# Optimization experiments

Hardware: AMD Instinct MI355X
Metric: run time of the kernel (lower is better)

Reference implementation:

```python
import jax, jax.numpy as jnp
import numpy as np

EPS = 1e-5

def _dynconv(x, w):
    # x: [B,C,H,W], w: [B,O,C,1,1] -> per-sample 1x1 conv == batched matmul
    return jnp.einsum('bchw,boc->bohw', x, w[:, :, :, 0, 0])

def _instance_norm(x):
    # InstanceNorm2d(affine=False): normalize over HxW per (b,c), biased var
    m = jnp.mean(x, axis=(2, 3), keepdims=True)
    v = jnp.var(x, axis=(2, 3), keepdims=True)
    return (x - m) / jnp.sqrt(v + EPS)

def setup_inputs() -> dict:
    key = jax.random.key(0)
    ks = jax.random.split(key, 10)
    B, C, O = 16, 128, 128
    hs = [128, 64, 32, 16, 8]
    inp = {}
    for i, h in enumerate(hs):
        inp[f'x{i+1}'] = jax.random.normal(ks[i], (B, C, h, h), dtype=jnp.float32)
        inp[f'l{i+1}fs'] = jax.random.normal(ks[5 + i], (B, O, C, 1, 1), dtype=jnp.float32)
    return inp

def reference(x1, x2, x3, x4, x5, l1fs, l2fs, l3fs, l4fs, l5fs):
    y1 = _instance_norm(_dynconv(x1, l1fs))
    y2 = _instance_norm(_dynconv(x2, l2fs))
    y3 = _instance_norm(_dynconv(x3, l3fs))
    y4 = _instance_norm(_dynconv(x4, l4fs))
    y5 = _dynconv(x5, l5fs)  # x5 is not normalized in the original
    return (y1, y2, y3, y4, y5)
```

## Files before the change

### kernel.cpp

```cpp
#include <hip/hip_runtime.h>
#include <hip/hip_bf16.h>

typedef float f32x4 __attribute__((ext_vector_type(4)));
typedef short s16x8 __attribute__((ext_vector_type(8)));
typedef short s16x4 __attribute__((ext_vector_type(4)));

static __device__ __forceinline__ short f2bf(float f) {
  union { __hip_bfloat16 h; short s; } u;
  u.h = __float2bfloat16(f);
  return u.s;
}
static __device__ __forceinline__ float bf2f(short s) {
  union { unsigned u; float f; } v;
  v.u = ((unsigned)(unsigned short)s) << 16;
  return v.f;
}
static __device__ __forceinline__ unsigned pack2(float a, float b) {
  return ((unsigned)(unsigned short)f2bf(a)) | (((unsigned)(unsigned short)f2bf(b)) << 16);
}
static __device__ __forceinline__ s16x8 pack8(f32x4 v0, f32x4 v1) {
  s16x8 r;
  r[0] = f2bf(v0.x); r[1] = f2bf(v0.y); r[2] = f2bf(v0.z); r[3] = f2bf(v0.w);
  r[4] = f2bf(v1.x); r[5] = f2bf(v1.y); r[6] = f2bf(v1.z); r[7] = f2bf(v1.w);
  return r;
}

#define GRAW_SZ   (4 * 16 * 16384)
#define MX_BASE   GRAW_SZ
#define MX_SZ     (4 * 16 * 128)
#define MEAN_BASE (MX_BASE + MX_SZ)
#define RSTD_BASE (MEAN_BASE + MX_SZ)

__global__ __launch_bounds__(256, 3) void k_gram(
    const float* __restrict__ x0, const float* __restrict__ x1,
    const float* __restrict__ x2, const float* __restrict__ x3,
    float* __restrict__ graw, float* __restrict__ mxraw) {
  const int bid = blockIdx.x;
  const float* xp; int s, b, ch, L; long long N;
  if (bid < 512)      { s = 0; b = bid >> 5; ch = bid & 31; xp = x0; N = 16384; L = 512; }
  else if (bid < 640) { int r = bid - 512; s = 1; b = r >> 3; ch = r & 7; xp = x1; N = 4096; L = 512; }
  else if (bid < 672) { int r = bid - 640; s = 2; b = r >> 1; ch = r & 1; xp = x2; N = 1024; L = 512; }
  else                { int r = bid - 672; s = 3; b = r;      ch = 0;     xp = x3; N = 256;  L = 256; }
  const int rounds = L >> 5;
  const int t = threadIdx.x;
  const int lane = t & 63, wv = t >> 6;
  const int wm = wv >> 1, wn = wv & 1;
  const int l15 = lane & 15, quad = lane >> 4;

  f32x4 acc[4][4];
  #pragma unroll
  for (int i = 0; i < 4; ++i)
    #pragma unroll
    for (int j = 0; j < 4; ++j) { f32x4 z = {0.f,0.f,0.f,0.f}; acc[i][j] = z; }
  float mxp[4] = {0.f, 0.f, 0.f, 0.f};

  const float* xb = xp + (long long)b * 128 * N + (long long)ch * L;
  const float* aptr[4]; const float* bptr[4];
  #pragma unroll
  for (int i = 0; i < 4; ++i)
    aptr[i] = xb + (long long)(wm * 64 + i * 16 + l15) * N + quad * 8;
  #pragma unroll
  for (int j = 0; j < 4; ++j)
    bptr[j] = xb + (long long)(wn * 64 + j * 16 + l15) * N + quad * 8;

  for (int r = 0; r < rounds; ++r) {
    const int k0 = r << 5;
    s16x8 af[4], bfq[4];
    #pragma unroll
    for (int i = 0; i < 4; ++i) {
      f32x4 v0 = *(const f32x4*)(aptr[i] + k0);
      f32x4 v1 = *(const f32x4*)(aptr[i] + k0 + 4);
      if (wn == 0)
        mxp[i] += (v0.x + v0.y + v0.z + v0.w) + (v1.x + v1.y + v1.z + v1.w);
      af[i] = pack8(v0, v1);
    }
    if (wm == wn) {
      #pragma unroll
      for (int j = 0; j < 4; ++j) bfq[j] = af[j];
    } else {
      #pragma unroll
      for (int j = 0; j < 4; ++j) {
        f32x4 v0 = *(const f32x4*)(bptr[j] + k0);
        f32x4 v1 = *(const f32x4*)(bptr[j] + k0 + 4);
        bfq[j] = pack8(v0, v1);
      }
    }
    #pragma unroll
    for (int i = 0; i < 4; ++i)
      #pragma unroll
      for (int j = 0; j < 4; ++j)
        acc[i][j] = __builtin_amdgcn_mfma_f32_16x16x32_bf16(af[i], bfq[j], acc[i][j], 0, 0, 0);
  }

  float* G = graw + (long long)(s * 16 + b) * 16384;
  #pragma unroll
  for (int i = 0; i < 4; ++i) {
    #pragma unroll
    for (int rr = 0; rr < 4; ++rr) {
      const int row = wm * 64 + i * 16 + quad * 4 + rr;
      #pragma unroll
      for (int j = 0; j < 4; ++j) {
        const int col = wn * 64 + j * 16 + l15;
        unsafeAtomicAdd(&G[row * 128 + col], acc[i][j][rr]);
      }
    }
  }
  #pragma unroll
  for (int i = 0; i < 4; ++i) {
    mxp[i] += __shfl_xor(mxp[i], 16, 64);
    mxp[i] += __shfl_xor(mxp[i], 32, 64);
  }
  if (wn == 0 && quad == 0) {
    float* MX = mxraw + (long long)(s * 16 + b) * 128;
    #pragma unroll
    for (int i = 0; i < 4; ++i)
      unsafeAtomicAdd(&MX[wm * 64 + i * 16 + l15], mxp[i]);
  }
}

__global__ __launch_bounds__(256) void k_stats(
    const float* __restrict__ l0, const float* __restrict__ l1,
    const float* __restrict__ l2, const float* __restrict__ l3,
    const float* __restrict__ graw, const float* __restrict__ mxraw,
    float* __restrict__ meanw, float* __restrict__ rstdw) {
  const int bid = blockIdx.x;
  const int s = bid >> 6, rm = bid & 63, b = rm >> 2, og = rm & 3;
  const float* lp = (s == 0) ? l0 : (s == 1) ? l1 : (s == 2) ? l2 : l3;
  const float Ninv = (s == 0) ? (1.f/16384.f) : (s == 1) ? (1.f/4096.f)
                   : (s == 2) ? (1.f/1024.f) : (1.f/256.f);
  const int t = threadIdx.x;

  __shared__ short Gs[16384];
  __shared__ float wl[32 * 132];
  __shared__ float mxl[128];
  __shared__ float red[4][32];
  __shared__ float meanb[32];

  const float* Gg = graw + (long long)(s * 16 + b) * 16384;
  #pragma unroll
  for (int jj = 0; jj < 16; ++jj) {
    const int F = jj * 256 + t;
    const int c = F >> 5, c4 = F & 31;
    f32x4 v = *(const f32x4*)(Gg + F * 4);
    const int q = c4 >> 1, half = c4 & 1;
    s16x4 sv; sv.x = f2bf(v.x); sv.y = f2bf(v.y); sv.z = f2bf(v.z); sv.w = f2bf(v.w);
    *(s16x4*)&Gs[c * 128 + ((q ^ (c & 15)) << 3) + half * 4] = sv;
  }
  const float* wg = lp + ((long long)b * 128 + og * 32) * 128;
  #pragma unroll
  for (int jj = 0; jj < 4; ++jj) {
    const int F = jj * 256 + t;
    const int o = F >> 5, c4 = F & 31;
    *(f32x4*)&wl[o * 132 + c4 * 4] = *(const f32x4*)(wg + F * 4);
  }
  if (t < 32) *(f32x4*)&mxl[t * 4] =
      *(const f32x4*)(mxraw + (long long)(s * 16 + b) * 128 + t * 4);
  __syncthreads();

  const int lane = t & 63, wv = t >> 6;
  const int oslot = lane >> 3, c8 = lane & 7;
  float e2a[4] = {0.f, 0.f, 0.f, 0.f};
  #pragma unroll
  for (int qq = 0; qq < 4; ++qq) {
    const int q = wv * 4 + qq;
    float wr[4][8];
    #pragma unroll
    for (int r = 0; r < 4; ++r) {
      f32x4 w0 = *(const f32x4*)&wl[(oslot + 8 * r) * 132 + q * 8];
      f32x4 w1 = *(const f32x4*)&wl[(oslot + 8 * r) * 132 + q * 8 + 4];
      wr[r][0]=w0.x; wr[r][1]=w0.y; wr[r][2]=w0.z; wr[r][3]=w0.w;
      wr[r][4]=w1.x; wr[r][5]=w1.y; wr[r][6]=w1.z; wr[r][7]=w1.w;
    }
    #pragma unroll
    for (int ci = 0; ci < 16; ++ci) {
      const int c = c8 + 8 * ci;
      s16x8 gv = *(const s16x8*)&Gs[c * 128 + ((q ^ (c & 15)) << 3)];
      float gf[8];
      #pragma unroll
      for (int k = 0; k < 8; ++k) gf[k] = bf2f(gv[k]);
      #pragma unroll
      for (int r = 0; r < 4; ++r) {
        float inner = 0.f;
        #pragma unroll
        for (int k = 0; k < 8; ++k) inner += wr[r][k] * gf[k];
        e2a[r] += wl[(oslot + 8 * r) * 132 + c] * inner;
      }
    }
  }
  float mn[4] = {0.f, 0.f, 0.f, 0.f};
  if (wv == 0) {
    #pragma unroll
    for (int ci = 0; ci < 16; ++ci) {
      const int c = c8 + 8 * ci;
      const float mxc = mxl[c];
      #pragma unroll
      for (int r = 0; r < 4; ++r) mn[r] += wl[(oslot + 8 * r) * 132 + c] * mxc;
    }
  }
  #pragma unroll
  for (int off = 1; off < 8; off <<= 1) {
    #pragma unroll
    for (int r = 0; r < 4; ++r) {
      e2a[r] += __shfl_xor(e2a[r], off, 64);
      mn[r]  += __shfl_xor(mn[r], off, 64);
    }
  }
  if (c8 == 0) {
    #pragma unroll
    for (int r = 0; r < 4; ++r) {
      red[wv][oslot + 8 * r] = e2a[r];
      if (wv == 0) meanb[oslot + 8 * r] = mn[r];
    }
  }
  __syncthreads();
  if (t < 32) {
    const float e2 = (red[0][t] + red[1][t] + red[2][t] + red[3][t]) * Ninv;
    const float mean = meanb[t] * Ninv;
    const float var = e2 - mean * mean;
    const float rstd = rsqrtf(var + 1e-5f);
    const int idx = (s * 16 + b) * 128 + og * 32 + t;
    meanw[idx] = mean;
    rstdw[idx] = rstd;
  }
}

__global__ __launch_bounds__(256, 3) void k_gemm(
    const float* __restrict__ x0, const float* __restrict__ x1,
    const float* __restrict__ x2, const float* __restrict__ x3,
    const float* __restrict__ x4,
    const float* __restrict__ l0, const float* __restrict__ l1,
    const float* __restrict__ l2, const float* __restrict__ l3,
    const float* __restrict__ l4,
    const float* __restrict__ meanw, const float* __restrict__ rstdw,
    float* __restrict__ out) {
  const int bid = blockIdx.x;
  int s, b, nt; const float *xp, *lp; int N; long long ooff;
  if (bid < 2048)      { s = 0; b = bid >> 7;            nt = bid & 127;     xp = x0; lp = l0; N = 16384; ooff = 0; }
  else if (bid < 2560) { int r = bid - 2048; s = 1; b = r >> 5; nt = r & 31; xp = x1; lp = l1; N = 4096;  ooff = 33554432LL; }
  else if (bid < 2688) { int r = bid - 2560; s = 2; b = r >> 3; nt = r & 7;  xp = x2; lp = l2; N = 1024;  ooff = 41943040LL; }
  else if (bid < 2720) { int r = bid - 2688; s = 3; b = r >> 1; nt = r & 1;  xp = x3; lp = l3; N = 256;   ooff = 44040192LL; }
  else                 { int r = bid - 2720; s = 4; b = r;      nt = 0;      xp = x4; lp = l4; N = 64;    ooff = 44564480LL; }
  const int t = threadIdx.x;
  const int lane = t & 63, wv = t >> 6;

  __shared__ short Xt[128 * 136];

  {
    const int g = lane >> 2, q4 = lane & 3;
    const float* xg = xp + (long long)b * 128 * N + (long long)nt * 128;
    #pragma unroll
    for (int j = 0; j < 16; ++j) {
      const int cb = (j & 7) * 16 + wv * 4;
      const int c  = cb + q4;
      const int n0 = (j >> 3) * 64 + g * 4;
      f32x4 v = {0.f, 0.f, 0.f, 0.f};
      if (nt * 128 + n0 + 3 < N)
        v = *(const f32x4*)(xg + (long long)c * N + n0);
      unsigned u01 = pack2(v.x, v.y);
      unsigned u23 = pack2(v.z, v.w);
      unsigned p01 = __shfl_xor(u01, 1, 64);
      unsigned p23 = __shfl_xor(u23, 1, 64);
      unsigned t01 = (q4 & 1) ? ((p01 >> 16) | (u01 & 0xffff0000u))
                              : ((u01 & 0xffffu) | (p01 << 16));
      unsigned t23 = (q4 & 1) ? ((p23 >> 16) | (u23 & 0xffff0000u))
                              : ((u23 & 0xffffu) | (p23 << 16));
      unsigned s01 = __shfl_xor(t01, 2, 64);
      unsigned s23 = __shfl_xor(t23, 2, 64);
      unsigned lo = (q4 & 2) ? s23 : t01;
      unsigned hi = (q4 & 2) ? t23 : s01;
      const int n = n0 + q4;
      *(unsigned long long*)&Xt[n * 136 + cb] =
          ((unsigned long long)hi << 32) | (unsigned long long)lo;
    }
  }
  __syncthreads();

  const int wm = wv >> 1, wn = wv & 1;
  const int l15 = lane & 15, quad = lane >> 4;
  const float* wg = lp + (long long)b * 16384;
  f32x4 acc[4][4];
  #pragma unroll
  for (int i = 0; i < 4; ++i)
    #pragma unroll
    for (int j = 0; j < 4; ++j) { f32x4 z = {0.f,0.f,0.f,0.f}; acc[i][j] = z; }

  #pragma unroll
  for (int kk = 0; kk < 4; ++kk) {
    s16x8 af[4], bfq[4];
    #pragma unroll
    for (int i = 0; i < 4; ++i) {
      const int m = wm * 64 + i * 16 + l15;
      f32x4 w0 = *(const f32x4*)(wg + m * 128 + kk * 32 + quad * 8);
      f32x4 w1 = *(const f32x4*)(wg + m * 128 + kk * 32 + quad * 8 + 4);
      af[i] = pack8(w0, w1);
    }
    #pragma unroll
    for (int j = 0; j < 4; ++j) {
      const int n = wn * 64 + j * 16 + l15;
      bfq[j] = *(const s16x8*)&Xt[n * 136 + kk * 32 + quad * 8];
    }
    #pragma unroll
    for (int i = 0; i < 4; ++i)
      #pragma unroll
      for (int j = 0; j < 4; ++j)
        acc[i][j] = __builtin_amdgcn_mfma_f32_16x16x32_bf16(af[i], bfq[j], acc[i][j], 0, 0, 0);
  }

  const int sb = (s * 16 + b) * 128;
  #pragma unroll
  for (int i = 0; i < 4; ++i) {
    #pragma unroll
    for (int rr = 0; rr < 4; ++rr) {
      const int o = wm * 64 + i * 16 + quad * 4 + rr;
      float mean = 0.f, rstd = 1.f;
      if (s < 4) { mean = meanw[sb + o]; rstd = rstdw[sb + o]; }
      float* orow = out + ooff + (long long)(b * 128 + o) * N + (long long)nt * 128;
      #pragma unroll
      for (int j = 0; j < 4; ++j) {
        const int n = wn * 64 + j * 16 + l15;
        if (nt * 128 + n < N) orow[n] = (acc[i][j][rr] - mean) * rstd;
      }
    }
  }
}

extern "C" void kernel_launch(void* const* d_in, const int* in_sizes, int n_in,
                              void* d_out, int out_size, void* d_ws, size_t ws_size,
                              hipStream_t stream) {
  const float* x[5] = {(const float*)d_in[0], (const float*)d_in[2], (const float*)d_in[4],
                       (const float*)d_in[6], (const float*)d_in[8]};
  const float* l[5] = {(const float*)d_in[1], (const float*)d_in[3], (const float*)d_in[5],
                       (const float*)d_in[7], (const float*)d_in[9]};
  float* ws  = (float*)d_ws;
  float* out = (float*)d_out;

  hipMemsetAsync(d_ws, 0, (size_t)(GRAW_SZ + MX_SZ) * sizeof(float), stream);

  k_gram <<<688,  256, 0, stream>>>(x[0], x[1], x[2], x[3], ws, ws + MX_BASE);
  k_stats<<<256,  256, 0, stream>>>(l[0], l[1], l[2], l[3], ws, ws + MX_BASE,
                                    ws + MEAN_BASE, ws + RSTD_BASE);
  k_gemm <<<2736, 256, 0, stream>>>(x[0], x[1], x[2], x[3], x[4],
                                    l[0], l[1], l[2], l[3], l[4],
                                    ws + MEAN_BASE, ws + RSTD_BASE, out);
}
```

Measured before the change: 459.1 us.

## Stage bf16 tiles in LDS for Gram kernel instead of direct global loads

The Gram kernel now loads a 128x128 chunk of X cooperatively with coalesced float4 reads, converts it to bf16 and stores it in padded shared memory. MFMA operands are then read from LDS, so off-diagonal waves no longer re-read the same rows from global memory in a scattered pattern. Row sums for the mean are now computed from the bf16-rounded values, which slightly changes precision. The change adds about 34KB of LDS per block and extra barriers, and nothing overlaps the loads with compute.

```diff
diff --git a/kernel.cpp b/kernel.cpp
--- a/kernel.cpp
+++ b/kernel.cpp
@@ -41,12 +41,14 @@
   else if (bid < 640) { int r = bid - 512; s = 1; b = r >> 3; ch = r & 7; xp = x1; N = 4096; L = 512; }
   else if (bid < 672) { int r = bid - 640; s = 2; b = r >> 1; ch = r & 1; xp = x2; N = 1024; L = 512; }
   else                { int r = bid - 672; s = 3; b = r;      ch = 0;     xp = x3; N = 256;  L = 256; }
-  const int rounds = L >> 5;
+  const int nsc = L >> 7;
   const int t = threadIdx.x;
   const int lane = t & 63, wv = t >> 6;
   const int wm = wv >> 1, wn = wv & 1;
   const int l15 = lane & 15, quad = lane >> 4;
 
+  __shared__ short Xs[128 * 136];
+
   f32x4 acc[4][4];
   #pragma unroll
   for (int i = 0; i < 4; ++i)
@@ -55,41 +57,53 @@
   float mxp[4] = {0.f, 0.f, 0.f, 0.f};
 
   const float* xb = xp + (long long)b * 128 * N + (long long)ch * L;
-  const float* aptr[4]; const float* bptr[4];
-  #pragma unroll
-  for (int i = 0; i < 4; ++i)
-    aptr[i] = xb + (long long)(wm * 64 + i * 16 + l15) * N + quad * 8;
-  #pragma unroll
-  for (int j = 0; j < 4; ++j)
-    bptr[j] = xb + (long long)(wn * 64 + j * 16 + l15) * N + quad * 8;
-
-  for (int r = 0; r < rounds; ++r) {
-    const int k0 = r << 5;
-    s16x8 af[4], bfq[4];
-    #pragma unroll
-    for (int i = 0; i < 4; ++i) {
-      f32x4 v0 = *(const f32x4*)(aptr[i] + k0);
-      f32x4 v1 = *(const f32x4*)(aptr[i] + k0 + 4);
-      if (wn == 0)
-        mxp[i] += (v0.x + v0.y + v0.z + v0.w) + (v1.x + v1.y + v1.z + v1.w);
-      af[i] = pack8(v0, v1);
-    }
-    if (wm == wn) {
-      #pragma unroll
-      for (int j = 0; j < 4; ++j) bfq[j] = af[j];
-    } else {
-      #pragma unroll
-      for (int j = 0; j < 4; ++j) {
-        f32x4 v0 = *(const f32x4*)(bptr[j] + k0);
-        f32x4 v1 = *(const f32x4*)(bptr[j] + k0 + 4);
-        bfq[j] = pack8(v0, v1);
-      }
-    }
-    #pragma unroll
-    for (int i = 0; i < 4; ++i)
-      #pragma unroll
-      for (int j = 0; j < 4; ++j)
-        acc[i][j] = __builtin_amdgcn_mfma_f32_16x16x32_bf16(af[i], bfq[j], acc[i][j], 0, 0, 0);
+
+  for (int sc = 0; sc < nsc; ++sc) {
+    if (sc) __syncthreads();
+    {
+      const int cg = t >> 5, kq = t & 31;
+      const float* gp = xb + (long long)sc * 128 + (long long)cg * N + (kq << 2);
+      short* lsp = &Xs[cg * 136 + (kq << 2)];
+      #pragma unroll
+      for (int it = 0; it < 16; ++it) {
+        f32x4 v = *(const f32x4*)gp;
+        s16x4 sv; sv[0]=f2bf(v.x); sv[1]=f2bf(v.y); sv[2]=f2bf(v.z); sv[3]=f2bf(v.w);
+        *(s16x4*)lsp = sv;
+        gp += (long long)8 * N;
+        lsp += 8 * 136;
+      }
+    }
+    __syncthreads();
+    #pragma unroll
+    for (int r4 = 0; r4 < 4; ++r4) {
+      const int k0 = (r4 << 5) + (quad << 3);
+      s16x8 af[4], bfq[4];
+      #pragma unroll
+      for (int i = 0; i < 4; ++i)
+        af[i] = *(const s16x8*)&Xs[(wm * 64 + i * 16 + l15) * 136 + k0];
+      if (wn == 0) {
+        #pragma unroll
+        for (int i = 0; i < 4; ++i) {
+          float sum8 = 0.f;
+          #pragma unroll
+          for (int k = 0; k < 8; ++k) sum8 += bf2f(af[i][k]);
+          mxp[i] += sum8;
+        }
+      }
+      if (wm == wn) {
+        #pragma unroll
+        for (int j = 0; j < 4; ++j) bfq[j] = af[j];
+      } else {
+        #pragma unroll
+        for (int j = 0; j < 4; ++j)
+          bfq[j] = *(const s16x8*)&Xs[(wn * 64 + j * 16 + l15) * 136 + k0];
+      }
+      #pragma unroll
+      for (int i = 0; i < 4; ++i)
+        #pragma unroll
+        for (int j = 0; j < 4; ++j)
+          acc[i][j] = __builtin_amdgcn_mfma_f32_16x16x32_bf16(af[i], bfq[j], acc[i][j], 0, 0, 0);
+    }
   }
 
   float* G = graw + (long long)(s * 16 + b) * 16384;
```

Result: no change. 451.4 us (-1.7%).

## Replace Gram-matrix statistics with fused epilogue stats and separate normalization pass

Applied to the files above, without the earlier changes.

The Gram-matrix pre-pass (k_gram plus k_stats), which re-read the inputs to predict the per-channel mean and variance, is removed. The GEMM epilogue now accumulates per-output-channel sum and sum of squares with wave shuffles and atomics, and writes unnormalized outputs. A small kernel turns these sums into mean and rstd, and a grid-stride kernel then normalizes the output in place. This drops the second read of the inputs and the Gram compute, but adds a full read-modify-write pass over the output, more atomics, and a one-pass variance formula that can lose precision.

```diff
diff --git a/kernel.cpp b/kernel.cpp
--- a/kernel.cpp
+++ b/kernel.cpp
@@ -9,11 +9,6 @@
   union { __hip_bfloat16 h; short s; } u;
   u.h = __float2bfloat16(f);
   return u.s;
-}
-static __device__ __forceinline__ float bf2f(short s) {
-  union { unsigned u; float f; } v;
-  v.u = ((unsigned)(unsigned short)s) << 16;
-  return v.f;
 }
 static __device__ __forceinline__ unsigned pack2(float a, float b) {
   return ((unsigned)(unsigned short)f2bf(a)) | (((unsigned)(unsigned short)f2bf(b)) << 16);
@@ -25,204 +20,9 @@
   return r;
 }
 
-#define GRAW_SZ   (4 * 16 * 16384)
-#define MX_BASE   GRAW_SZ
-#define MX_SZ     (4 * 16 * 128)
-#define MEAN_BASE (MX_BASE + MX_SZ)
-#define RSTD_BASE (MEAN_BASE + MX_SZ)
-
-__global__ __launch_bounds__(256, 3) void k_gram(
-    const float* __restrict__ x0, const float* __restrict__ x1,
-    const float* __restrict__ x2, const float* __restrict__ x3,
-    float* __restrict__ graw, float* __restrict__ mxraw) {
-  const int bid = blockIdx.x;
-  const float* xp; int s, b, ch, L; long long N;
-  if (bid < 512)      { s = 0; b = bid >> 5; ch = bid & 31; xp = x0; N = 16384; L = 512; }
-  else if (bid < 640) { int r = bid - 512; s = 1; b = r >> 3; ch = r & 7; xp = x1; N = 4096; L = 512; }
-  else if (bid < 672) { int r = bid - 640; s = 2; b = r >> 1; ch = r & 1; xp = x2; N = 1024; L = 512; }
-  else                { int r = bid - 672; s = 3; b = r;      ch = 0;     xp = x3; N = 256;  L = 256; }
-  const int rounds = L >> 5;
-  const int t = threadIdx.x;
-  const int lane = t & 63, wv = t >> 6;
-  const int wm = wv >> 1, wn = wv & 1;
-  const int l15 = lane & 15, quad = lane >> 4;
-
-  f32x4 acc[4][4];
-  #pragma unroll
-  for (int i = 0; i < 4; ++i)
-    #pragma unroll
-    for (int j = 0; j < 4; ++j) { f32x4 z = {0.f,0.f,0.f,0.f}; acc[i][j] = z; }
-  float mxp[4] = {0.f, 0.f, 0.f, 0.f};
-
-  const float* xb = xp + (long long)b * 128 * N + (long long)ch * L;
-  const float* aptr[4]; const float* bptr[4];
-  #pragma unroll
-  for (int i = 0; i < 4; ++i)
-    aptr[i] = xb + (long long)(wm * 64 + i * 16 + l15) * N + quad * 8;
-  #pragma unroll
-  for (int j = 0; j < 4; ++j)
-    bptr[j] = xb + (long long)(wn * 64 + j * 16 + l15) * N + quad * 8;
-
-  for (int r = 0; r < rounds; ++r) {
-    const int k0 = r << 5;
-    s16x8 af[4], bfq[4];
-    #pragma unroll
-    for (int i = 0; i < 4; ++i) {
-      f32x4 v0 = *(const f32x4*)(aptr[i] + k0);
-      f32x4 v1 = *(const f32x4*)(aptr[i] + k0 + 4);
-      if (wn == 0)
-        mxp[i] += (v0.x + v0.y + v0.z + v0.w) + (v1.x + v1.y + v1.z + v1.w);
-      af[i] = pack8(v0, v1);
-    }
-    if (wm == wn) {
-      #pragma unroll
-      for (int j = 0; j < 4; ++j) bfq[j] = af[j];
-    } else {
-      #pragma unroll
-      for (int j = 0; j < 4; ++j) {
-        f32x4 v0 = *(const f32x4*)(bptr[j] + k0);
-        f32x4 v1 = *(const f32x4*)(bptr[j] + k0 + 4);
-        bfq[j] = pack8(v0, v1);
-      }
-    }
-    #pragma unroll
-    for (int i = 0; i < 4; ++i)
-      #pragma unroll
-      for (int j = 0; j < 4; ++j)
-        acc[i][j] = __builtin_amdgcn_mfma_f32_16x16x32_bf16(af[i], bfq[j], acc[i][j], 0, 0, 0);
-  }
-
-  float* G = graw + (long long)(s * 16 + b) * 16384;
-  #pragma unroll
-  for (int i = 0; i < 4; ++i) {
-    #pragma unroll
-    for (int rr = 0; rr < 4; ++rr) {
-      const int row = wm * 64 + i * 16 + quad * 4 + rr;
-      #pragma unroll
-      for (int j = 0; j < 4; ++j) {
-        const int col = wn * 64 + j * 16 + l15;
-        unsafeAtomicAdd(&G[row * 128 + col], acc[i][j][rr]);
-      }
-    }
-  }
-  #pragma unroll
-  for (int i = 0; i < 4; ++i) {
-    mxp[i] += __shfl_xor(mxp[i], 16, 64);
-    mxp[i] += __shfl_xor(mxp[i], 32, 64);
-  }
-  if (wn == 0 && quad == 0) {
-    float* MX = mxraw + (long long)(s * 16 + b) * 128;
-    #pragma unroll
-    for (int i = 0; i < 4; ++i)
-      unsafeAtomicAdd(&MX[wm * 64 + i * 16 + l15], mxp[i]);
-  }
-}
-
-__global__ __launch_bounds__(256) void k_stats(
-    const float* __restrict__ l0, const float* __restrict__ l1,
-    const float* __restrict__ l2, const float* __restrict__ l3,
-    const float* __restrict__ graw, const float* __restrict__ mxraw,
-    float* __restrict__ meanw, float* __restrict__ rstdw) {
-  const int bid = blockIdx.x;
-  const int s = bid >> 6, rm = bid & 63, b = rm >> 2, og = rm & 3;
-  const float* lp = (s == 0) ? l0 : (s == 1) ? l1 : (s == 2) ? l2 : l3;
-  const float Ninv = (s == 0) ? (1.f/16384.f) : (s == 1) ? (1.f/4096.f)
-                   : (s == 2) ? (1.f/1024.f) : (1.f/256.f);
-  const int t = threadIdx.x;
-
-  __shared__ short Gs[16384];
-  __shared__ float wl[32 * 132];
-  __shared__ float mxl[128];
-  __shared__ float red[4][32];
-  __shared__ float meanb[32];
-
-  const float* Gg = graw + (long long)(s * 16 + b) * 16384;
-  #pragma unroll
-  for (int jj = 0; jj < 16; ++jj) {
-    const int F = jj * 256 + t;
-    const int c = F >> 5, c4 = F & 31;
-    f32x4 v = *(const f32x4*)(Gg + F * 4);
-    const int q = c4 >> 1, half = c4 & 1;
-    s16x4 sv; sv.x = f2bf(v.x); sv.y = f2bf(v.y); sv.z = f2bf(v.z); sv.w = f2bf(v.w);
-    *(s16x4*)&Gs[c * 128 + ((q ^ (c & 15)) << 3) + half * 4] = sv;
-  }
-  const float* wg = lp + ((long long)b * 128 + og * 32) * 128;
-  #pragma unroll
-  for (int jj = 0; jj < 4; ++jj) {
-    const int F = jj * 256 + t;
-    const int o = F >> 5, c4 = F & 31;
-    *(f32x4*)&wl[o * 132 + c4 * 4] = *(const f32x4*)(wg + F * 4);
-  }
-  if (t < 32) *(f32x4*)&mxl[t * 4] =
-      *(const f32x4*)(mxraw + (long long)(s * 16 + b) * 128 + t * 4);
-  __syncthreads();
-
-  const int lane = t & 63, wv = t >> 6;
-  const int oslot = lane >> 3, c8 = lane & 7;
-  float e2a[4] = {0.f, 0.f, 0.f, 0.f};
-  #pragma unroll
-  for (int qq = 0; qq < 4; ++qq) {
-    const int q = wv * 4 + qq;
-    float wr[4][8];
-    #pragma unroll
-    for (int r = 0; r < 4; ++r) {
-      f32x4 w0 = *(const f32x4*)&wl[(oslot + 8 * r) * 132 + q * 8];
-      f32x4 w1 = *(const f32x4*)&wl[(oslot + 8 * r) * 132 + q * 8 + 4];
-      wr[r][0]=w0.x; wr[r][1]=w0.y; wr[r][2]=w0.z; wr[r][3]=w0.w;
-      wr[r][4]=w1.x; wr[r][5]=w1.y; wr[r][6]=w1.z; wr[r][7]=w1.w;
-    }
-    #pragma unroll
-    for (int ci = 0; ci < 16; ++ci) {
-      const int c = c8 + 8 * ci;
-      s16x8 gv = *(const s16x8*)&Gs[c * 128 + ((q ^ (c & 15)) << 3)];
-      float gf[8];
-      #pragma unroll
-      for (int k = 0; k < 8; ++k) gf[k] = bf2f(gv[k]);
-      #pragma unroll
-      for (int r = 0; r < 4; ++r) {
-        float inner = 0.f;
-        #pragma unroll
-        for (int k = 0; k < 8; ++k) inner += wr[r][k] * gf[k];
-        e2a[r] += wl[(oslot + 8 * r) * 132 + c] * inner;
-      }
-    }
-  }
-  float mn[4] = {0.f, 0.f, 0.f, 0.f};
-  if (wv == 0) {
-    #pragma unroll
-    for (int ci = 0; ci < 16; ++ci) {
-      const int c = c8 + 8 * ci;
-      const float mxc = mxl[c];
-      #pragma unroll
-      for (int r = 0; r < 4; ++r) mn[r] += wl[(oslot + 8 * r) * 132 + c] * mxc;
-    }
-  }
-  #pragma unroll
-  for (int off = 1; off < 8; off <<= 1) {
-    #pragma unroll
-    for (int r = 0; r < 4; ++r) {
-      e2a[r] += __shfl_xor(e2a[r], off, 64);
-      mn[r]  += __shfl_xor(mn[r], off, 64);
-    }
-  }
-  if (c8 == 0) {
-    #pragma unroll
-    for (int r = 0; r < 4; ++r) {
-      red[wv][oslot + 8 * r] = e2a[r];
-      if (wv == 0) meanb[oslot + 8 * r] = mn[r];
-    }
-  }
-  __syncthreads();
-  if (t < 32) {
-    const float e2 = (red[0][t] + red[1][t] + red[2][t] + red[3][t]) * Ninv;
-    const float mean = meanb[t] * Ninv;
-    const float var = e2 - mean * mean;
-    const float rstd = rsqrtf(var + 1e-5f);
-    const int idx = (s * 16 + b) * 128 + og * 32 + t;
-    meanw[idx] = mean;
-    rstdw[idx] = rstd;
-  }
-}
+#define STAT_SZ   (4 * 16 * 128 * 2)
+#define MEAN_BASE STAT_SZ
+#define RSTD_BASE (MEAN_BASE + 4 * 16 * 128)
 
 __global__ __launch_bounds__(256, 3) void k_gemm(
     const float* __restrict__ x0, const float* __restrict__ x1,
@@ -231,8 +31,7 @@
     const float* __restrict__ l0, const float* __restrict__ l1,
     const float* __restrict__ l2, const float* __restrict__ l3,
     const float* __restrict__ l4,
-    const float* __restrict__ meanw, const float* __restrict__ rstdw,
-    float* __restrict__ out) {
+    float* __restrict__ stat, float* __restrict__ out) {
   const int bid = blockIdx.x;
   int s, b, nt; const float *xp, *lp; int N; long long ooff;
   if (bid < 2048)      { s = 0; b = bid >> 7;            nt = bid & 127;     xp = x0; lp = l0; N = 16384; ooff = 0; }
@@ -306,21 +105,80 @@
         acc[i][j] = __builtin_amdgcn_mfma_f32_16x16x32_bf16(af[i], bfq[j], acc[i][j], 0, 0, 0);
   }
 
-  const int sb = (s * 16 + b) * 128;
+  if (s < 4) {
+    float* ST = stat + (long long)(s * 16 + b) * 256;
+    #pragma unroll
+    for (int i = 0; i < 4; ++i) {
+      #pragma unroll
+      for (int rr = 0; rr < 4; ++rr) {
+        float sv = 0.f, sq = 0.f;
+        #pragma unroll
+        for (int j = 0; j < 4; ++j) {
+          const float v = acc[i][j][rr];
+          sv += v; sq += v * v;
+        }
+        #pragma unroll
+        for (int off = 1; off < 16; off <<= 1) {
+          sv += __shfl_xor(sv, off, 64);
+          sq += __shfl_xor(sq, off, 64);
+        }
+        if (l15 == 0) {
+          const int o = wm * 64 + i * 16 + quad * 4 + rr;
+          unsafeAtomicAdd(&ST[o * 2],     sv);
+          unsafeAtomicAdd(&ST[o * 2 + 1], sq);
+        }
+      }
+    }
+  }
+
   #pragma unroll
   for (int i = 0; i < 4; ++i) {
     #pragma unroll
     for (int rr = 0; rr < 4; ++rr) {
       const int o = wm * 64 + i * 16 + quad * 4 + rr;
-      float mean = 0.f, rstd = 1.f;
-      if (s < 4) { mean = meanw[sb + o]; rstd = rstdw[sb + o]; }
       float* orow = out + ooff + (long long)(b * 128 + o) * N + (long long)nt * 128;
       #pragma unroll
       for (int j = 0; j < 4; ++j) {
         const int n = wn * 64 + j * 16 + l15;
-        if (nt * 128 + n < N) orow[n] = (acc[i][j][rr] - mean) * rstd;
+        if (nt * 128 + n < N) orow[n] = acc[i][j][rr];
       }
     }
+  }
+}
+
+__global__ __launch_bounds__(256) void k_final(
+    const float* __restrict__ stat, float* __restrict__ meanw,
+    float* __restrict__ rstdw) {
+  const int idx = blockIdx.x * 256 + threadIdx.x;
+  const int s = idx >> 11;
+  const float Ninv = (s == 0) ? (1.f/16384.f) : (s == 1) ? (1.f/4096.f)
+                   : (s == 2) ? (1.f/1024.f) : (1.f/256.f);
+  const float sv = stat[idx * 2], sq = stat[idx * 2 + 1];
+  const float mean = sv * Ninv;
+  const float var  = sq * Ninv - mean * mean;
+  meanw[idx] = mean;
+  rstdw[idx] = rsqrtf(var + 1e-5f);
+}
+
+__global__ __launch_bounds__(256) void k_norm(
+    const float* __restrict__ meanw, const float* __restrict__ rstdw,
+    float* __restrict__ out) {
+  const long long V = 11141120LL;
+  const long long stride = (long long)gridDim.x * 256;
+  for (long long v = (long long)blockIdx.x * 256 + threadIdx.x; v < V; v += stride) {
+    const long long e = v << 2;
+    int mi;
+    if (e < 33554432LL)      mi =        (int)(e >> 14);
+    else if (e < 41943040LL) mi = 2048 + (int)((e - 33554432LL) >> 12);
+    else if (e < 44040192LL) mi = 4096 + (int)((e - 41943040LL) >> 10);
+    else                     mi = 6144 + (int)((e - 44040192LL) >> 8);
+    const float mean = meanw[mi], rstd = rstdw[mi];
+    f32x4 y = *(const f32x4*)(out + e);
+    y.x = (y.x - mean) * rstd;
+    y.y = (y.y - mean) * rstd;
+    y.z = (y.z - mean) * rstd;
+    y.w = (y.w - mean) * rstd;
+    *(f32x4*)(out + e) = y;
   }
 }
 
@@ -334,12 +192,11 @@
   float* ws  = (float*)d_ws;
   float* out = (float*)d_out;
 
-  hipMemsetAsync(d_ws, 0, (size_t)(GRAW_SZ + MX_SZ) * sizeof(float), stream);
-
-  k_gram <<<688,  256, 0, stream>>>(x[0], x[1], x[2], x[3], ws, ws + MX_BASE);
-  k_stats<<<256,  256, 0, stream>>>(l[0], l[1], l[2], l[3], ws, ws + MX_BASE,
-                                    ws + MEAN_BASE, ws + RSTD_BASE);
+  hipMemsetAsync(d_ws, 0, (size_t)STAT_SZ * sizeof(float), stream);
+
   k_gemm <<<2736, 256, 0, stream>>>(x[0], x[1], x[2], x[3], x[4],
                                     l[0], l[1], l[2], l[3], l[4],
-                                    ws + MEAN_BASE, ws + RSTD_BASE, out);
-}
+                                    ws, out);
+  k_final<<<32,   256, 0, stream>>>(ws, ws + MEAN_BASE, ws + RSTD_BASE);
+  k_norm <<<2048, 256, 0, stream>>>(ws + MEAN_BASE, ws + RSTD_BASE, out);
+}
```

Measured after the change: 547.5 us. +19.3%, slower.
